# Optimization experiments

Hardware: AMD Instinct MI355X
Metric: run time of the kernel (lower is better)

## Reference

```python
import jax, jax.numpy as jnp
import numpy as np

NUM_ELEMENTS = 14
EMPTY_ID, WALL_ID = 0, 1
# 8-neighborhood direction offsets (dy, dx); DIRS[(a+4)%8] == -DIRS[a]
DIRS = [(-1, 0), (-1, 1), (0, 1), (1, 1), (1, 0), (1, -1), (0, -1), (-1, -1)]


def shift(x, a):
    """out[..., i, j] = x[..., i+dy, j+dx] with zero padding at borders (pw.direction_func)."""
    dy, dx = DIRS[a]
    B, C, H, W = x.shape
    xp = jnp.pad(x, ((0, 0), (0, 0), (1, 1), (1, 1)))
    return jax.lax.slice(xp, (0, 0, 1 + dy, 1 + dx), (B, C, 1 + dy + H, 1 + dx + W))


def setup_inputs() -> dict:
    key = jax.random.key(0)
    k1, k2 = jax.random.split(key)
    B, C, H, W = 4, NUM_ELEMENTS + 6, 512, 512
    world = jax.random.uniform(k1, (B, C, H, W), dtype=jnp.float32)
    velocity_field = jax.random.normal(k2, (B, 2, H, W), dtype=jnp.float32)
    elem_empty = jnp.zeros((C,), dtype=jnp.float32).at[EMPTY_ID].set(1.0)
    return {"world": world, "velocity_field": velocity_field, "elem_empty": elem_empty}


def reference(world, velocity_field, elem_empty):
    dtype = world.dtype
    empty_vec = elem_empty[None, :, None, None]  # [1, C, 1, 1]
    inv_2pi = 1.0 / (2.0 * np.pi)

    for _ in range(2):
        mag = jnp.linalg.norm(velocity_field, axis=1, keepdims=True)  # [B,1,H,W]
        raw = inv_2pi * jnp.arccos(velocity_field[:, 1:2] / (mag + 0.001))
        ang = jnp.where(velocity_field[:, 0:1] < 0, 1.0 - raw, raw)
        bucket = jnp.mod(jnp.floor(ang * 8.0 + 0.5), 8.0)
        vel_enough = mag > 0.1
        vdelta = velocity_field
        for a in range(8):
            opp = (a + 4) % 8
            empty_b = world[:, EMPTY_ID:EMPTY_ID + 1] > 0.5
            wall_b = world[:, WALL_ID:WALL_ID + 1] > 0.5
            is_match = bucket == a
            is_empty_dir = shift(empty_b, a) & (~wall_b)
            sa = is_match & vel_enough & is_empty_dir          # does_become_empty
            sb = shift(sa, opp)                                 # does_become_opposite
            saf = sa.astype(dtype)
            sbf = sb.astype(dtype)
            opp_world = shift(world, opp)
            # interp_vel: world - sa*world - sb*world + sa*empty_vec + sb*opp_world
            world = world - saf * world - sbf * world + saf * empty_vec + sbf * opp_world
            opp_vel = shift(velocity_field, opp)
            vdelta = vdelta - saf * velocity_field * 0.5 + sbf * opp_vel * 0.5
        velocity_field = vdelta

    velocity_field = velocity_field * 0.95
    kernel = jnp.ones((1, 1, 3, 3), dtype) / 18.0

    def smooth(ch):  # ch: [B,1,H,W]
        conv = jax.lax.conv_general_dilated(
            ch, kernel, window_strides=(1, 1), padding=((1, 1), (1, 1)),
            dimension_numbers=("NCHW", "OIHW", "NCHW"))
        return conv + ch * 0.5

    velocity_field = jnp.concatenate(
        [smooth(velocity_field[:, 0:1]), smooth(velocity_field[:, 1:2])], axis=1)
    world = world.at[:, NUM_ELEMENTS + 4:NUM_ELEMENTS + 6].set(velocity_field)
    return world, velocity_field
```

## Files before the change

kernel.cpp:

```cpp
#include <hip/hip_runtime.h>
#include <math.h>

#define HH 512
#define WW 512
#define HW (HH*WW)
#define BATCH 4
#define NCH 18
#define BHW (BATCH*HW)

__device__ __constant__ int cDG[8] = {-512,-511,1,513,512,511,-1,-513};
__device__ __constant__ int cDT[8] = {-48,-47,1,49,48,47,-1,-49};

__global__ __launch_bounds__(256) void bv_bucket_kernel(
    const float* __restrict__ vel, unsigned char* __restrict__ bk,
    unsigned* __restrict__ pcount)
{
    int idx = blockIdx.x*256 + threadIdx.x;
    if (idx == 0) { pcount[0] = 0; pcount[1] = 0; }
    if (idx >= BHW) return;
    int b = idx >> 18;
    int rem = idx & (HW-1);
    const float* vb = vel + (size_t)b*2*HW;
    float vy = vb[rem];
    float vx = vb[HW + rem];
    float a2 = vy*vy;
    float b2 = vx*vx;
    float mag = sqrtf(a2 + b2);
    float xx = vx / (mag + 0.001f);
    float af = (float)acos((double)xx);
    const float inv2pi = (float)(1.0/(2.0*3.14159265358979323846));
    float raw = inv2pi * af;
    float ang = (vy < 0.0f) ? (1.0f - raw) : raw;
    float t = ang * 8.0f + 0.5f;
    int bkt = (int)floorf(t);
    bkt &= 7;
    unsigned char e = (mag > 0.1f) ? (unsigned char)8 : (unsigned char)0;
    bk[idx] = (unsigned char)(bkt | e);
}

#define ATP 48
#define ATC (48*48)
#define ANT 512
#define PAD 49

template<bool COMPOSE>
__global__ __launch_bounds__(ANT) void bv_mask_kernel(
    const float* __restrict__ Win, int Cin,
    float* __restrict__ Wout, int Cout,
    const unsigned char* __restrict__ bkall,
    unsigned short* __restrict__ MSg,
    int* __restrict__ SrcOut,
    const float* __restrict__ velg,
    float* __restrict__ vdout,
    unsigned char* __restrict__ bkout,
    const int* __restrict__ Src1g,
    unsigned* __restrict__ pcount,
    uint2* __restrict__ tlist,
    unsigned listcap,
    const float* __restrict__ elem_empty)
{
    __shared__ __align__(16) unsigned char SHM[40864];
    float* A0  = ((float*)(SHM +     0)) + PAD;
    float* A1  = ((float*)(SHM +  9608)) + PAD;
    float* B0F = ((float*)(SHM + 19216)) + PAD;
    float* B1F = ((float*)(SHM + 28824)) + PAD;
    unsigned char* KSH = SHM + 38432 + PAD;
    unsigned* sCnt = (unsigned*)(SHM + 40840);

    unsigned char* MSHb = SHM + 19216 + PAD;
    unsigned char* SBb  = SHM + 28824 + PAD;

    const int tid = threadIdx.x;
    const int blk = blockIdx.x;
    const int tx = blk & 15, ty = (blk >> 4) & 15, b = blk >> 8;
    const int x0 = tx*32 - 8, y0 = ty*32 - 8;

    const float* inb  = Win  + (size_t)b*Cin*HW;
    float*       outb = Wout + (size_t)b*Cout*HW;
    const unsigned char* bkb = bkall + ((size_t)b << 18);
    unsigned short* MSob = MSg + ((size_t)b << 18);
    int*            Srb  = SrcOut + ((size_t)b << 18);
    const float* velb = velg  + (size_t)b*2*HW;
    float*       vdb  = vdout + (size_t)b*2*HW;

    const float e0 = elem_empty[0];
    const float e1 = elem_empty[1];

    float v0r[4], v1r[4];
    unsigned kreg[4], mreg[4];
    unsigned mtail = 0;

    if (tid == 0) sCnt[0] = 0;

    #pragma unroll
    for (int k = 0; k < 4; ++k) {
        int l = tid + (k << 9);
        int ly = l / ATP, lx = l - ly*ATP;
        int gy = y0 + ly, gx = x0 + lx;
        bool in = ((unsigned)gy < HH) && ((unsigned)gx < WW);
        int g = gy*WW + gx;
        float v0 = 0.f, v1 = 0.f; unsigned char kk = 0;
        if (in) { v0 = inb[g]; v1 = inb[HW + g]; kk = bkb[g]; }
        A0[l] = v0; A1[l] = v1; KSH[l] = kk;
        v0r[k] = v0; v1r[k] = v1; kreg[k] = kk; mreg[k] = 0;
    }
    if (tid < 256) {
        int l = 2048 + tid;
        int ly = l / ATP, lx = l - ly*ATP;
        int gy = y0 + ly, gx = x0 + lx;
        bool in = ((unsigned)gy < HH) && ((unsigned)gx < WW);
        int g = gy*WW + gx;
        float v0 = 0.f, v1 = 0.f; unsigned char kk = 0;
        if (in) { v0 = inb[g]; v1 = inb[HW + g]; kk = bkb[g]; }
        A0[l] = v0; A1[l] = v1; KSH[l] = kk;
    }
    __syncthreads();

    #pragma unroll
    for (int a = 0; a < 8; ++a) {
        const int doff = cDT[a];
        const unsigned tgt = (unsigned)(a | 8);
        const float* cA0 = (a & 1) ? B0F : A0;
        const float* cA1 = (a & 1) ? B1F : A1;
        float* nA0 = (a & 1) ? A0 : B0F;
        float* nA1 = (a & 1) ? A1 : B1F;
        #pragma unroll
        for (int k = 0; k < 4; ++k) {
            const int l = tid + (k << 9);
            const int ln = l + doff;
            const int lo = l - doff;
            float a0l = v0r[k], a1l = v1r[k];
            float a0n = cA0[ln];
            float a0o = cA0[lo], a1o = cA1[lo];
            unsigned ko = KSH[lo];
            bool sal = ((kreg[k] & 15u) == tgt) & (a0n > 0.5f) & !(a1l > 0.5f);
            bool sao = ((ko & 15u) == tgt) & (a0l > 0.5f) & !(a1o > 0.5f);
            mreg[k] |= (sal ? 1u : 0u) << a;
            float sa = sal ? 1.0f : 0.0f;
            float sb = sao ? 1.0f : 0.0f;
            float r0 = a0l - sa*a0l; r0 = r0 - sb*a0l; r0 = r0 + sa*e0; r0 = r0 + sb*a0o;
            float r1 = a1l - sa*a1l; r1 = r1 - sb*a1l; r1 = r1 + sa*e1; r1 = r1 + sb*a1o;
            v0r[k] = r0; v1r[k] = r1;
            nA0[l] = r0; nA1[l] = r1;
        }
        if (tid < 256) {
            const int l = 2048 + tid;
            const int ln = l + doff;
            const int lo = l - doff;
            float a0l = cA0[l], a1l = cA1[l];
            float a0n = cA0[ln];
            float a0o = cA0[lo], a1o = cA1[lo];
            unsigned kl = KSH[l], ko = KSH[lo];
            bool sal = ((kl & 15u) == tgt) & (a0n > 0.5f) & !(a1l > 0.5f);
            bool sao = ((ko & 15u) == tgt) & (a0l > 0.5f) & !(a1o > 0.5f);
            if (sal) mtail |= 1u << a;
            float sa = sal ? 1.0f : 0.0f;
            float sb = sao ? 1.0f : 0.0f;
            float r0 = a0l - sa*a0l; r0 = r0 - sb*a0l; r0 = r0 + sa*e0; r0 = r0 + sb*a0o;
            float r1 = a1l - sa*a1l; r1 = r1 - sb*a1l; r1 = r1 + sa*e1; r1 = r1 + sb*a1o;
            nA0[l] = r0; nA1[l] = r1;
        }
        __syncthreads();
    }

    #pragma unroll
    for (int k = 0; k < 4; ++k) MSHb[tid + (k << 9)] = (unsigned char)mreg[k];
    if (tid < 256) MSHb[2048 + tid] = (unsigned char)mtail;
    __syncthreads();

    for (int l = tid; l < ATC; l += ANT) {
        unsigned sb8 = 0;
        #pragma unroll
        for (int a = 0; a < 8; ++a) {
            int lo = l - cDT[a];
            sb8 |= (unsigned)((MSHb[lo] >> a) & 1) << a;
        }
        SBb[l] = (unsigned char)sb8;
    }
    __syncthreads();

    int tNeed[2]; unsigned tLL[2], tEy[2];
    #pragma unroll
    for (int it = 0; it < 2; ++it) {
        tNeed[it] = 0;
        int li = tid + (it << 9);
        int iy = li >> 5, ix = li & 31;
        int l = (iy + 8)*ATP + ix + 8;
        int gy = ty*32 + iy, gx = tx*32 + ix;
        int g = gy*WW + gx;
        outb[g]      = A0[l];
        outb[HW + g] = A1[l];
        unsigned mm = MSHb[l], sbb = SBb[l];
        MSob[g] = (unsigned short)(mm | (sbb << 8));

        {
            float vy = velb[g], vx = velb[HW + g];
            float ddy = vy, ddx = vx;
            unsigned act = mm | sbb;
            if (act) {
                #pragma unroll
                for (int a = 0; a < 8; ++a) {
                    if ((act >> a) & 1) {
                        float sa = (float)((mm  >> a) & 1);
                        float sb = (float)((sbb >> a) & 1);
                        float voy = 0.f, vox = 0.f;
                        if (sb != 0.f) {
                            int go = g - cDG[a];
                            voy = velb[go]; vox = velb[HW + go];
                        }
                        ddy = ddy - (sa*vy)*0.5f; ddy = ddy + (sb*voy)*0.5f;
                        ddx = ddx - (sa*vx)*0.5f; ddx = ddx + (sb*vox)*0.5f;
                    }
                }
            }
            vdb[g]      = ddy;
            vdb[HW + g] = ddx;
            if constexpr (!COMPOSE) {
                float a2 = ddy*ddy;
                float b2 = ddx*ddx;
                float mag = sqrtf(a2 + b2);
                float xx = ddx / (mag + 0.001f);
                float af = (float)acos((double)xx);
                const float inv2pi = (float)(1.0/(2.0*3.14159265358979323846));
                float raw = inv2pi * af;
                float ang = (ddy < 0.0f) ? (1.0f - raw) : raw;
                float t = ang * 8.0f + 0.5f;
                int bkt = (int)floorf(t);
                bkt &= 7;
                unsigned char e = (mag > 0.1f) ? (unsigned char)8 : (unsigned char)0;
                bkout[((size_t)b << 18) + g] = (unsigned char)(bkt | e);
            }
        }

        int cc = l, ss = 7, kd = 0;
        unsigned m = mm, sb = sbb;
        while (true) {
            unsigned evt = (m | sb) & ((2u << ss) - 1u);
            if (!evt) { kd = 0; break; }
            int bb = 31 - __builtin_clz(evt);
            int ia = (m >> bb) & 1, ib = (sb >> bb) & 1;
            if (ia && ib) { kd = 2; break; }
            if (ia) { kd = 1; break; }
            cc -= cDT[bb]; ss = bb - 1;
            if (ss < 0) { kd = 0; break; }
            m = MSHb[cc]; sb = SBb[cc];
        }
        if (kd == 1) {
            Srb[g] = (int)(1u << 30);
        } else if (kd == 0) {
            int cly = cc / ATP, clx = cc - cly*ATP;
            unsigned s = (unsigned)((y0 + cly)*WW + (x0 + clx));
            if (!COMPOSE) {
                Srb[g] = (int)s;
            } else {
                unsigned r1 = (unsigned)Src1g[((size_t)b << 18) + s];
                unsigned k1 = r1 >> 30;
                if (k1 == 0u)      Srb[g] = (int)r1;
                else if (k1 == 1u) Srb[g] = (int)(1u << 30);
                else { tNeed[it] = 1; tEy[it] = s; }
            }
        } else {
            if (!COMPOSE) {
                Srb[g] = (int)(2u << 30);
            } else {
                int cly = cc / ATP, clx = cc - cly*ATP;
                unsigned ccg = (unsigned)((y0 + cly)*WW + (x0 + clx));
                tNeed[it] = 1;
                tEy[it] = (1u << 31) | ((unsigned)ss << 28) | ccg;
            }
        }
        if (COMPOSE && tNeed[it]) tLL[it] = atomicAdd(&sCnt[0], 1u);
    }
    if constexpr (COMPOSE) {
        __syncthreads();
        if (tid == 0) sCnt[1] = sCnt[0] ? atomicAdd(&pcount[1], sCnt[0]) : 0u;
        __syncthreads();
        unsigned lbase = sCnt[1];
        #pragma unroll
        for (int it = 0; it < 2; ++it) {
            if (!tNeed[it]) continue;
            int li = tid + (it << 9);
            int iy = li >> 5, ix = li & 31;
            int g = (ty*32 + iy)*WW + tx*32 + ix;
            unsigned lidx = lbase + tLL[it];
            if (lidx < listcap) {
                tlist[lidx] = make_uint2(((unsigned)b << 18) | (unsigned)g, tEy[it]);
                Srb[g] = (int)(2u << 30);
            } else {
                Srb[g] = (int)(3u << 30);
            }
        }
    }
}

__device__ __attribute__((noinline)) float bv_eval(
    int cell, int stp,
    const unsigned short* __restrict__ MS,
    const float* __restrict__ initc)
{
    float vstk[10]; int vsp = 0;
    int cs_cell[10], cs_stp[10], cs_ph[10]; int csp = 0;
    cs_cell[0] = cell; cs_stp[0] = stp; cs_ph[0] = 0; csp = 1;
    while (csp > 0) {
        int ph = cs_ph[csp-1];
        if (ph == 0) {
            int cc = cs_cell[csp-1], ss = cs_stp[csp-1];
            float result = 0.0f; int have = 0;
            while (true) {
                if (ss < 0) { result = initc[cc]; have = 1; break; }
                unsigned v = MS[cc];
                unsigned m = v & 255u, sb = v >> 8;
                unsigned evt = (m | sb) & ((2u << ss) - 1u);
                if (!evt) { result = initc[cc]; have = 1; break; }
                int bb = 31 - __builtin_clz(evt);
                int ia = (m >> bb) & 1, ib = (sb >> bb) & 1;
                if (ia && ib) {
                    cs_cell[csp-1] = cc; cs_stp[csp-1] = bb; cs_ph[csp-1] = 1;
                    cs_cell[csp] = cc - cDG[bb]; cs_stp[csp] = bb - 1; cs_ph[csp] = 0; csp++;
                    break;
                }
                if (ia) { result = 0.0f; have = 1; break; }
                cc -= cDG[bb]; ss = bb - 1;
            }
            if (have) { vstk[vsp++] = result; csp--; }
        } else if (ph == 1) {
            cs_ph[csp-1] = 2;
            cs_cell[csp] = cs_cell[csp-1]; cs_stp[csp] = cs_stp[csp-1] - 1;
            cs_ph[csp] = 0; csp++;
        } else {
            float Bv = vstk[--vsp]; float Av = vstk[--vsp];
            vstk[vsp++] = Av - Bv;
            csp--;
        }
    }
    return vstk[0];
}

__device__ float bv_leaf1_1(int L,
    const unsigned short* __restrict__ MS1,
    const float* __restrict__ ic)
{
    int cc = L, ss = 7;
    while (true) {
        unsigned v = MS1[cc];
        unsigned m = v & 255u, sb = v >> 8;
        unsigned evt = (m | sb) & ((2u << ss) - 1u);
        if (!evt) break;
        int bb = 31 - __builtin_clz(evt);
        int ia = (m >> bb) & 1, ib = (sb >> bb) & 1;
        if (ia && ib) return bv_eval(cc, bb, MS1, ic);
        if (ia) return 0.0f;
        cc -= cDG[bb]; ss = bb - 1;
        if (ss < 0) break;
    }
    return ic[cc];
}

__device__ float bv_eval1_ind(int cell, int stp,
    const unsigned short* __restrict__ MS2,
    const unsigned short* __restrict__ MS1,
    const float* __restrict__ ic)
{
    float vstk[10]; int vsp = 0;
    int cs_cell[10], cs_stp[10], cs_ph[10]; int csp = 0;
    cs_cell[0] = cell; cs_stp[0] = stp; cs_ph[0] = 0; csp = 1;
    while (csp > 0) {
        int ph = cs_ph[csp-1];
        if (ph == 0) {
            int cc = cs_cell[csp-1], ss = cs_stp[csp-1];
            int have = 0, zero = 0, leaf = 0;
            while (true) {
                if (ss < 0) { leaf = cc; have = 1; break; }
                unsigned v = MS2[cc];
                unsigned m = v & 255u, sb = v >> 8;
                unsigned evt = (m | sb) & ((2u << ss) - 1u);
                if (!evt) { leaf = cc; have = 1; break; }
                int bb = 31 - __builtin_clz(evt);
                int ia = (m >> bb) & 1, ib = (sb >> bb) & 1;
                if (ia && ib) {
                    cs_cell[csp-1] = cc; cs_stp[csp-1] = bb; cs_ph[csp-1] = 1;
                    cs_cell[csp] = cc - cDG[bb]; cs_stp[csp] = bb - 1; cs_ph[csp] = 0; csp++;
                    break;
                }
                if (ia) { zero = 1; have = 1; break; }
                cc -= cDG[bb]; ss = bb - 1;
            }
            if (have) {
                vstk[vsp++] = zero ? 0.0f : bv_leaf1_1(leaf, MS1, ic);
                csp--;
            }
        } else if (ph == 1) {
            cs_ph[csp-1] = 2;
            cs_cell[csp] = cs_cell[csp-1]; cs_stp[csp] = cs_stp[csp-1] - 1;
            cs_ph[csp] = 0; csp++;
        } else {
            float Bv = vstk[--vsp]; float Av = vstk[--vsp];
            vstk[vsp++] = Av - Bv;
            csp--;
        }
    }
    return vstk[0];
}

__global__ __launch_bounds__(256) void bv_apply_kernel(
    const float* __restrict__ Win, int Cin,
    float* __restrict__ Wout, int Cout,
    const int* __restrict__ Src)
{
    int t = blockIdx.x*256 + threadIdx.x;
    if (t >= BHW/8) return;
    const int c0 = 2 + blockIdx.y*4;
    int p = t << 3;
    int b = p >> 18;
    int own = p & (HW-1);
    const float* inb  = Win  + (size_t)b*Cin*HW;
    float*       outb = Wout + (size_t)b*Cout*HW;
    const int* Srb = Src + ((size_t)b << 18);

    int4 sA = *(const int4*)(Srb + own);
    int4 sB = *(const int4*)(Srb + own + 4);
    unsigned sv[8] = {(unsigned)sA.x, (unsigned)sA.y, (unsigned)sA.z, (unsigned)sA.w,
                      (unsigned)sB.x, (unsigned)sB.y, (unsigned)sB.z, (unsigned)sB.w};
    int kind[8], idx[8]; bool need[8];
    bool allself = true;
    #pragma unroll
    for (int j = 0; j < 8; ++j) {
        kind[j] = (int)(sv[j] >> 30);
        idx[j]  = (int)(sv[j] & 0x3FFFFu);
        need[j] = (kind[j] != 0) || (idx[j] != own + j);
        allself = allself && !need[j];
    }

    if (allself) {
        #pragma unroll
        for (int c = 0; c < 4; ++c) {
            const float* ic = inb + (size_t)(c0 + c)*HW;
            float*       oc = outb + (size_t)(c0 + c)*HW;
            float4 va = *(const float4*)(ic + own);
            float4 vb = *(const float4*)(ic + own + 4);
            *(float4*)(oc + own)     = va;
            *(float4*)(oc + own + 4) = vb;
        }
        return;
    }
    #pragma unroll
    for (int c = 0; c < 4; ++c) {
        const float* ic = inb + (size_t)(c0 + c)*HW;
        float*       oc = outb + (size_t)(c0 + c)*HW;
        float4 va = *(const float4*)(ic + own);
        float4 vb = *(const float4*)(ic + own + 4);
        float r[8] = {va.x, va.y, va.z, va.w, vb.x, vb.y, vb.z, vb.w};
        #pragma unroll
        for (int j = 0; j < 8; ++j) {
            if (need[j])
                r[j] = (kind[j] == 0) ? ic[idx[j]] : 0.0f;
        }
        *(float4*)(oc + own)     = make_float4(r[0], r[1], r[2], r[3]);
        *(float4*)(oc + own + 4) = make_float4(r[4], r[5], r[6], r[7]);
    }
}

__global__ __launch_bounds__(256) void bv_tree_kernel(
    const float* __restrict__ Win,
    float* __restrict__ Wout,
    const uint2* __restrict__ tlist,
    const unsigned* __restrict__ pcount,
    unsigned listcap,
    const unsigned short* __restrict__ MS1,
    const unsigned short* __restrict__ MS2)
{
    unsigned n = pcount[1]; if (n > listcap) n = listcap;
    unsigned total = n * 16;
    for (unsigned i = blockIdx.x*256 + threadIdx.x; i < total; i += gridDim.x*256) {
        unsigned ei = i >> 4; int c = 2 + (int)(i & 15);
        uint2 e = tlist[ei];
        int b = (int)((e.x >> 18) & 3u);
        int g = (int)(e.x & 0x3FFFFu);
        const float* ic = Win  + (size_t)b*20*HW + (size_t)c*HW;
        float*       oc = Wout + (size_t)b*20*HW + (size_t)c*HW;
        const unsigned short* MS1b = MS1 + ((size_t)b << 18);
        float r;
        if (e.y >> 31) {
            int cc = (int)(e.y & 0x3FFFFu);
            int ss = (int)((e.y >> 28) & 7u);
            const unsigned short* MS2b = MS2 + ((size_t)b << 18);
            r = bv_eval1_ind(cc, ss, MS2b, MS1b, ic);
        } else {
            int s = (int)(e.y & 0x3FFFFu);
            r = bv_leaf1_1(s, MS1b, ic);
        }
        oc[g] = r;
    }
}

__global__ __launch_bounds__(256) void bv_smooth_kernel(
    const float* __restrict__ vin, float* __restrict__ dout)
{
    int idx = blockIdx.x*256 + threadIdx.x;
    if (idx >= BATCH*2*HW) return;
    int x = idx & (WW-1);
    int y = (idx >> 9) & (HH-1);
    int c = (idx >> 18) & 1;
    int b = idx >> 19;
    const float* vb = vin + (size_t)(b*2 + c)*HW;
    const float w18 = (float)(1.0/18.0);
    float acc = 0.0f;
    for (int ky = -1; ky <= 1; ++ky) {
        int yy = y + ky;
        if ((unsigned)yy >= HH) continue;
        for (int kx = -1; kx <= 1; ++kx) {
            int xx2 = x + kx;
            if ((unsigned)xx2 >= WW) continue;
            float s = 0.95f * vb[yy*WW + xx2];
            acc += s * w18;
        }
    }
    float sc = 0.95f * vb[y*WW + x];
    float res = acc + sc * 0.5f;
    dout[((size_t)b*20 + 18 + c)*HW + (size_t)(y<<9) + x] = res;
    dout[(size_t)BATCH*20*HW + (size_t)idx] = res;
}

extern "C" void kernel_launch(void* const* d_in, const int* in_sizes, int n_in,
                              void* d_out, int out_size, void* d_ws, size_t ws_size,
                              hipStream_t stream)
{
    const float* world_in   = (const float*)d_in[0];
    const float* vel_in     = (const float*)d_in[1];
    const float* elem_empty = (const float*)d_in[2];
    float* out = (float*)d_out;

    float* w01  = (float*)d_ws;
    float* vd1  = w01 + (size_t)BATCH*2*HW;
    float* vel2 = vd1 + (size_t)BATCH*2*HW;
    unsigned char* bk  = (unsigned char*)(vel2 + (size_t)BATCH*2*HW);
    unsigned short* MS1 = (unsigned short*)(bk + (size_t)BHW);
    unsigned short* MS2 = MS1 + (size_t)BHW;
    int* Src1 = (int*)(MS2 + (size_t)BHW);
    int* Src2 = Src1 + (size_t)BHW;
    unsigned* pcount = (unsigned*)(Src2 + (size_t)BHW);
    uint2* tlistb = (uint2*)(pcount + 16);
    const unsigned listcap = 1u << 18;

    dim3 blk(256);
    dim3 grd((BHW + 255)/256);
    dim3 g2((BATCH*2*HW + 255)/256);
    dim3 gA(BATCH*16*16);
    dim3 gB(BHW/8/256, 4);
    dim3 gT(1024);

    bv_bucket_kernel<<<grd, blk, 0, stream>>>(vel_in, bk, pcount);
    bv_mask_kernel<false><<<gA, dim3(ANT), 0, stream>>>(
        world_in, 20, w01, 2, bk, MS1, Src1,
        vel_in, vd1, bk,
        (const int*)nullptr, pcount, (uint2*)nullptr, 0u, elem_empty);
    bv_mask_kernel<true><<<gA, dim3(ANT), 0, stream>>>(
        w01, 2, out, 20, bk, MS2, Src2,
        vd1, vel2, (unsigned char*)nullptr,
        Src1, pcount, tlistb, listcap, elem_empty);
    bv_apply_kernel<<<gB, blk, 0, stream>>>(world_in, 20, out, 20, Src2);
    bv_tree_kernel<<<gT, blk, 0, stream>>>(world_in, out, tlistb, pcount,
                                           listcap, MS1, MS2);
    bv_smooth_kernel<<<g2, blk, 0, stream>>>(vel2, out);
}
```

Baseline: 169.7 us.

## Split dual-branch tree evaluation across thread pairs and batch apply-kernel loads

Result: slower. 200.6 us (+18.2%).

```diff
diff --git a/kernel.cpp b/kernel.cpp
--- a/kernel.cpp
+++ b/kernel.cpp
@@ -443,20 +443,25 @@
         }
         return;
     }
+    float r[4][8];
     #pragma unroll
     for (int c = 0; c < 4; ++c) {
         const float* ic = inb + (size_t)(c0 + c)*HW;
-        float*       oc = outb + (size_t)(c0 + c)*HW;
         float4 va = *(const float4*)(ic + own);
         float4 vb = *(const float4*)(ic + own + 4);
-        float r[8] = {va.x, va.y, va.z, va.w, vb.x, vb.y, vb.z, vb.w};
+        r[c][0] = va.x; r[c][1] = va.y; r[c][2] = va.z; r[c][3] = va.w;
+        r[c][4] = vb.x; r[c][5] = vb.y; r[c][6] = vb.z; r[c][7] = vb.w;
         #pragma unroll
         for (int j = 0; j < 8; ++j) {
             if (need[j])
-                r[j] = (kind[j] == 0) ? ic[idx[j]] : 0.0f;
-        }
-        *(float4*)(oc + own)     = make_float4(r[0], r[1], r[2], r[3]);
-        *(float4*)(oc + own + 4) = make_float4(r[4], r[5], r[6], r[7]);
+                r[c][j] = (kind[j] == 0) ? ic[idx[j]] : 0.0f;
+        }
+    }
+    #pragma unroll
+    for (int c = 0; c < 4; ++c) {
+        float* oc = outb + (size_t)(c0 + c)*HW;
+        *(float4*)(oc + own)     = make_float4(r[c][0], r[c][1], r[c][2], r[c][3]);
+        *(float4*)(oc + own + 4) = make_float4(r[c][4], r[c][5], r[c][6], r[c][7]);
     }
 }
 
@@ -470,26 +475,41 @@
     const unsigned short* __restrict__ MS2)
 {
     unsigned n = pcount[1]; if (n > listcap) n = listcap;
-    unsigned total = n * 16;
+    unsigned total = n * 32;
     for (unsigned i = blockIdx.x*256 + threadIdx.x; i < total; i += gridDim.x*256) {
-        unsigned ei = i >> 4; int c = 2 + (int)(i & 15);
+        unsigned ei = i >> 5;
+        int c = 2 + (int)((i >> 1) & 15);
+        int h = (int)(i & 1);
         uint2 e = tlist[ei];
         int b = (int)((e.x >> 18) & 3u);
         int g = (int)(e.x & 0x3FFFFu);
         const float* ic = Win  + (size_t)b*20*HW + (size_t)c*HW;
         float*       oc = Wout + (size_t)b*20*HW + (size_t)c*HW;
         const unsigned short* MS1b = MS1 + ((size_t)b << 18);
-        float r;
+        float val = 0.0f;
         if (e.y >> 31) {
             int cc = (int)(e.y & 0x3FFFFu);
             int ss = (int)((e.y >> 28) & 7u);
             const unsigned short* MS2b = MS2 + ((size_t)b << 18);
-            r = bv_eval1_ind(cc, ss, MS2b, MS1b, ic);
+            unsigned v = MS2b[cc];
+            unsigned m = v & 255u, sb = v >> 8;
+            unsigned evt = (m | sb) & ((2u << ss) - 1u);
+            bool dual = false; int bb = 0;
+            if (evt) {
+                bb = 31 - __builtin_clz(evt);
+                dual = (((m >> bb) & 1) != 0) && (((sb >> bb) & 1) != 0);
+            }
+            if (dual) {
+                if (h == 0) val = bv_eval1_ind(cc - cDG[bb], bb - 1, MS2b, MS1b, ic);
+                else        val = bv_eval1_ind(cc, bb - 1, MS2b, MS1b, ic);
+            } else if (h == 0) {
+                val = bv_eval1_ind(cc, ss, MS2b, MS1b, ic);
+            }
         } else {
-            int s = (int)(e.y & 0x3FFFFu);
-            r = bv_leaf1_1(s, MS1b, ic);
-        }
-        oc[g] = r;
+            if (h == 0) val = bv_leaf1_1((int)(e.y & 0x3FFFFu), MS1b, ic);
+        }
+        float partner = __shfl_xor(val, 1);
+        if (h == 0) oc[g] = val - partner;
     }
 }
 
@@ -547,7 +567,7 @@
     dim3 g2((BATCH*2*HW + 255)/256);
     dim3 gA(BATCH*16*16);
     dim3 gB(BHW/8/256, 4);
-    dim3 gT(1024);
+    dim3 gT(2048);
 
     bv_bucket_kernel<<<grd, blk, 0, stream>>>(vel_in, bk, pcount);
     bv_mask_kernel<false><<<gA, dim3(ANT), 0, stream>>>(
```
